# Kernel optimization log

Hardware: AMD Instinct MI355X
Metric: run time of the kernel (lower is better)

The kernel has to match this reference:

```python
import jax, jax.numpy as jnp
import numpy as np

B, T, D, H, HD, FF = 1024, 128, 128, 4, 32, 512
SCALE = D ** -0.5  # NOTE: original scales by full EMBED_DIM**-0.5, not head_dim
EPS = 1e-5


def setup_inputs() -> dict:
    key = jax.random.key(0)
    ks = jax.random.split(key, 14)
    s = 0.02
    return {
        "x": jax.random.normal(ks[0], (B, T, D), dtype=jnp.float32),
        "ln1_g": jnp.ones((D,), jnp.float32),
        "ln1_b": jnp.zeros((D,), jnp.float32),
        "Wq": jax.random.normal(ks[1], (H, HD, D), jnp.float32) * s,
        "Wk": jax.random.normal(ks[2], (H, HD, D), jnp.float32) * s,
        "Wv": jax.random.normal(ks[3], (H, HD, D), jnp.float32) * s,
        "Wo": jax.random.normal(ks[4], (D, D), jnp.float32) * s,
        "bo": jnp.zeros((D,), jnp.float32),
        "ln2_g": jnp.ones((D,), jnp.float32),
        "ln2_b": jnp.zeros((D,), jnp.float32),
        "W1": jax.random.normal(ks[5], (FF, D), jnp.float32) * s,
        "b1": jnp.zeros((FF,), jnp.float32),
        "W2": jax.random.normal(ks[6], (D, FF), jnp.float32) * s,
        "b2": jnp.zeros((D,), jnp.float32),
    }


def _layer_norm(x, g, b):
    mu = jnp.mean(x, axis=-1, keepdims=True)
    var = jnp.mean(jnp.square(x - mu), axis=-1, keepdims=True)
    return (x - mu) * jax.lax.rsqrt(var + EPS) * g + b


def reference(x, ln1_g, ln1_b, Wq, Wk, Wv, Wo, bo, ln2_g, ln2_b, W1, b1, W2, b2):
    # --- attention sub-block ---
    h = _layer_norm(x, ln1_g, ln1_b)                       # [B,T,D]
    q = jnp.einsum('btd,nhd->bnth', h, Wq)                 # [B,H,T,HD]
    k = jnp.einsum('btd,nhd->bnth', h, Wk)
    v = jnp.einsum('btd,nhd->bnth', h, Wv)
    scores = jnp.einsum('bnth,bnsh->bnts', q, k) * SCALE   # [B,H,T,T]
    causal = jnp.tril(jnp.ones((T, T), dtype=bool))
    scores = jnp.where(causal, scores, -jnp.inf)
    w = jax.nn.softmax(scores, axis=-1)                    # dropout = eval identity
    attn = jnp.einsum('bnts,bnsh->bnth', w, v)             # [B,H,T,HD]
    attn = attn.transpose(0, 2, 1, 3).reshape(B, T, D)     # concat heads
    x = x + attn @ Wo.T + bo
    # --- feed-forward sub-block ---
    h2 = _layer_norm(x, ln2_g, ln2_b)
    ff = jax.nn.relu(h2 @ W1.T + b1) @ W2.T + b2
    return x + ff
```

## Files before the change

kernel.cpp:

```cpp
#include <hip/hip_runtime.h>
#include <hip/hip_bf16.h>


typedef short bf16x8 __attribute__((ext_vector_type(8)));
typedef float f32x4  __attribute__((ext_vector_type(4)));
typedef unsigned short u16;
typedef unsigned int   u32;

#define TT   128
#define DDIM 128
#define FFD  512
#define PIT  136

#define QSC 0.12751744f

#if defined(__has_builtin)
#if __has_builtin(__builtin_amdgcn_exp2f)
#define EXP2F(x) __builtin_amdgcn_exp2f(x)
#else
#define EXP2F(x) exp2f(x)
#endif
#else
#define EXP2F(x) exp2f(x)
#endif

__device__ __forceinline__ u16 f2b(float f) {
    __hip_bfloat16 h = __float2bfloat16(f);
    return __builtin_bit_cast(u16, h);
}
__device__ __forceinline__ u32 pk2(float x, float y) {
    return (u32)f2b(x) | ((u32)f2b(y) << 16);
}
__device__ __forceinline__ void st_b64(u16* p, u32 lo, u32 hi) {
    uint2 v; v.x = lo; v.y = hi;
    *reinterpret_cast<uint2*>(p) = v;
}
__device__ __forceinline__ bf16x8 ldfrag(const u16* p) {
    return __builtin_bit_cast(bf16x8, *reinterpret_cast<const uint4*>(p));
}
__device__ __forceinline__ bf16x8 ldfrag_f32(const float* p) {
    float4 a = *reinterpret_cast<const float4*>(p);
    float4 b = *reinterpret_cast<const float4*>(p + 4);
    bf16x8 r;
    r[0] = (short)f2b(a.x); r[1] = (short)f2b(a.y);
    r[2] = (short)f2b(a.z); r[3] = (short)f2b(a.w);
    r[4] = (short)f2b(b.x); r[5] = (short)f2b(b.y);
    r[6] = (short)f2b(b.z); r[7] = (short)f2b(b.w);
    return r;
}
__device__ __forceinline__ f32x4 mfma16(bf16x8 a, bf16x8 b, f32x4 c) {
    return __builtin_amdgcn_mfma_f32_16x16x32_bf16(a, b, c, 0, 0, 0);
}

__global__ __launch_bounds__(512, 2) void tblock_kernel(
    const float* __restrict__ x,
    const float* __restrict__ ln1g, const float* __restrict__ ln1b,
    const float* __restrict__ Wq,   const float* __restrict__ Wk, const float* __restrict__ Wv,
    const float* __restrict__ Wo,   const float* __restrict__ bo,
    const float* __restrict__ ln2g, const float* __restrict__ ln2b,
    const float* __restrict__ W1,   const float* __restrict__ b1,
    const float* __restrict__ W2,   const float* __restrict__ b2,
    float* __restrict__ out)
{
    __shared__ __align__(16) u16 sm[4 * TT * PIT];
    u16* bufA = sm;
    u16* bufB = sm + 1 * TT * PIT;
    u16* bufC = sm + 2 * TT * PIT;
    u16* bufD = sm + 3 * TT * PIT;

    const int b    = blockIdx.x;
    const int tid  = threadIdx.x;
    const int w    = tid >> 6;
    const int l    = tid & 63;
    const int lq   = l & 15;
    const int quad = l >> 4;
    const float* xb = x + (size_t)b * (TT * DDIM);

    {
        const int row = tid >> 2, part = tid & 3;
        const float* src = xb + row * DDIM + part * 32;
        float v[32];
        float s = 0.f, s2 = 0.f;
        #pragma unroll
        for (int i = 0; i < 8; i++) {
            float4 u = *reinterpret_cast<const float4*>(src + i * 4);
            v[i * 4 + 0] = u.x; v[i * 4 + 1] = u.y;
            v[i * 4 + 2] = u.z; v[i * 4 + 3] = u.w;
            s  += u.x + u.y + u.z + u.w;
            s2 += u.x * u.x + u.y * u.y + u.z * u.z + u.w * u.w;
        }
        s  += __shfl_xor(s, 1);  s2 += __shfl_xor(s2, 1);
        s  += __shfl_xor(s, 2);  s2 += __shfl_xor(s2, 2);
        float mean = s * (1.f / 128.f);
        float var  = fmaxf(s2 * (1.f / 128.f) - mean * mean, 0.f);
        float rstd = rsqrtf(var + 1e-5f);
        u16* dst = bufA + row * PIT + part * 32;
        #pragma unroll
        for (int i = 0; i < 4; i++) {
            u32 o4[4];
            #pragma unroll
            for (int j = 0; j < 4; j++) {
                int c = part * 32 + i * 8 + 2 * j;
                float r0 = (v[i * 8 + 2 * j]     - mean) * rstd * ln1g[c]     + ln1b[c];
                float r1 = (v[i * 8 + 2 * j + 1] - mean) * rstd * ln1g[c + 1] + ln1b[c + 1];
                o4[j] = (u32)f2b(r0) | ((u32)f2b(r1) << 16);
            }
            uint4 pk; pk.x = o4[0]; pk.y = o4[1]; pk.z = o4[2]; pk.w = o4[3];
            *reinterpret_cast<uint4*>(dst + i * 8) = pk;
        }
    }
    __syncthreads();

    {
        bf16x8 aq[4], ak[4];
        #pragma unroll
        for (int ks = 0; ks < 4; ks++) {
            aq[ks] = ldfrag_f32(Wq + (w * 16 + lq) * DDIM + ks * 32 + quad * 8);
            ak[ks] = ldfrag_f32(Wk + (w * 16 + lq) * DDIM + ks * 32 + quad * 8);
        }
        #pragma unroll
        for (int m = 0; m < 8; m++) {
            f32x4 accq = {0, 0, 0, 0}, acck = {0, 0, 0, 0};
            #pragma unroll
            for (int ks = 0; ks < 4; ks++) {
                bf16x8 bh = ldfrag(bufA + (m * 16 + lq) * PIT + ks * 32 + quad * 8);
                accq = mfma16(aq[ks], bh, accq);
                acck = mfma16(ak[ks], bh, acck);
            }
            int t = m * 16 + lq;
            st_b64(bufB + t * PIT + w * 16 + quad * 4, pk2(accq[0], accq[1]), pk2(accq[2], accq[3]));
            st_b64(bufC + t * PIT + w * 16 + quad * 4, pk2(acck[0], acck[1]), pk2(acck[2], acck[3]));
        }
        bf16x8 av[4];
        #pragma unroll
        for (int ks = 0; ks < 4; ks++)
            av[ks] = ldfrag_f32(Wv + (w * 16 + lq) * DDIM + ks * 32 + quad * 8);
        #pragma unroll
        for (int n = 0; n < 8; n++) {
            f32x4 acc = {0, 0, 0, 0};
            #pragma unroll
            for (int ks = 0; ks < 4; ks++) {
                bf16x8 bh = ldfrag(bufA + (n * 16 + lq) * PIT + ks * 32 + quad * 8);
                acc = mfma16(av[ks], bh, acc);
            }
            #pragma unroll
            for (int r = 0; r < 4; r++) {
                int o = w * 16 + quad * 4 + r;
                bufD[o * PIT + n * 16 + lq] = f2b(acc[r]);
            }
        }
    }
    __syncthreads();

    const int trow = w * 16 + lq;
    #pragma unroll 1
    for (int h = 0; h < 4; h++) {
        bf16x8 qb = ldfrag(bufB + trow * PIT + h * 32 + quad * 8);
        float p[8][4];
        #pragma unroll
        for (int n = 0; n < 8; n++) {
            bf16x8 ka = ldfrag(bufC + (n * 16 + lq) * PIT + h * 32 + quad * 8);
            f32x4 s4 = mfma16(ka, qb, f32x4{0, 0, 0, 0});
            #pragma unroll
            for (int r = 0; r < 4; r++) p[n][r] = s4[r];
        }
        float mx = -3.0e38f;
        #pragma unroll
        for (int n = 0; n < 8; n++) {
            #pragma unroll
            for (int r = 0; r < 4; r++) {
                int sc = n * 16 + quad * 4 + r;
                float q = p[n][r] * QSC;
                p[n][r] = q;
                mx = (sc <= trow) ? fmaxf(mx, q) : mx;
            }
        }
        mx = fmaxf(mx, __shfl_xor(mx, 16));
        mx = fmaxf(mx, __shfl_xor(mx, 32));
        float sum = 0.f;
        #pragma unroll
        for (int n = 0; n < 8; n++) {
            float e[4];
            #pragma unroll
            for (int r = 0; r < 4; r++) {
                int sc = n * 16 + quad * 4 + r;
                e[r] = (sc <= trow) ? EXP2F(p[n][r] - mx) : 0.f;
                sum += e[r];
            }
            st_b64(bufA + trow * PIT + n * 16 + quad * 4, pk2(e[0], e[1]), pk2(e[2], e[3]));
        }
        sum += __shfl_xor(sum, 16);
        sum += __shfl_xor(sum, 32);
        float inv = 1.f / sum;
        asm volatile("s_waitcnt lgkmcnt(0)" ::: "memory");
        __builtin_amdgcn_sched_barrier(0);
        f32x4 o0 = {0, 0, 0, 0}, o1 = {0, 0, 0, 0};
        #pragma unroll
        for (int ks = 0; ks < 4; ks++) {
            bf16x8 pb  = ldfrag(bufA + trow * PIT + ks * 32 + quad * 8);
            bf16x8 va0 = ldfrag(bufD + (h * 32 + lq) * PIT + ks * 32 + quad * 8);
            bf16x8 va1 = ldfrag(bufD + (h * 32 + 16 + lq) * PIT + ks * 32 + quad * 8);
            o0 = mfma16(va0, pb, o0);
            o1 = mfma16(va1, pb, o1);
        }
        #pragma unroll
        for (int r = 0; r < 4; r++) { o0[r] *= inv; o1[r] *= inv; }
        st_b64(bufB + trow * PIT + h * 32 + quad * 4,      pk2(o0[0], o0[1]), pk2(o0[2], o0[3]));
        st_b64(bufB + trow * PIT + h * 32 + 16 + quad * 4, pk2(o1[0], o1[1]), pk2(o1[2], o1[3]));
    }
    __syncthreads();

    float x1res[8][4];
    {
        bf16x8 woa[4];
        #pragma unroll
        for (int ks = 0; ks < 4; ks++)
            woa[ks] = ldfrag_f32(Wo + (w * 16 + lq) * DDIM + ks * 32 + quad * 8);
        const float4 bo4 = *reinterpret_cast<const float4*>(bo + w * 16 + quad * 4);
        #pragma unroll
        for (int m = 0; m < 8; m++) {
            f32x4 acc = {0, 0, 0, 0};
            #pragma unroll
            for (int ks = 0; ks < 4; ks++) {
                bf16x8 ab = ldfrag(bufB + (m * 16 + lq) * PIT + ks * 32 + quad * 8);
                acc = mfma16(woa[ks], ab, acc);
            }
            int t = m * 16 + lq;
            const float4 xv = *reinterpret_cast<const float4*>(xb + t * DDIM + w * 16 + quad * 4);
            float v0 = acc[0] + xv.x + bo4.x;
            float v1 = acc[1] + xv.y + bo4.y;
            float v2 = acc[2] + xv.z + bo4.z;
            float v3 = acc[3] + xv.w + bo4.w;
            x1res[m][0] = v0; x1res[m][1] = v1; x1res[m][2] = v2; x1res[m][3] = v3;
            st_b64(bufC + t * PIT + w * 16 + quad * 4, pk2(v0, v1), pk2(v2, v3));
        }
    }
    __syncthreads();

    {
        const int row = tid >> 2, part = tid & 3;
        const u16* src = bufC + row * PIT + part * 32;
        float v[32];
        float s = 0.f, s2 = 0.f;
        #pragma unroll
        for (int i = 0; i < 4; i++) {
            uint4 u = *reinterpret_cast<const uint4*>(src + i * 8);
            u32 arr[4] = {u.x, u.y, u.z, u.w};
            #pragma unroll
            for (int j = 0; j < 4; j++) {
                float f0 = __uint_as_float((arr[j] & 0xffffu) << 16);
                float f1 = __uint_as_float(arr[j] & 0xffff0000u);
                v[i * 8 + 2 * j] = f0; v[i * 8 + 2 * j + 1] = f1;
                s += f0 + f1; s2 += f0 * f0 + f1 * f1;
            }
        }
        s  += __shfl_xor(s, 1);  s2 += __shfl_xor(s2, 1);
        s  += __shfl_xor(s, 2);  s2 += __shfl_xor(s2, 2);
        float mean = s * (1.f / 128.f);
        float var  = fmaxf(s2 * (1.f / 128.f) - mean * mean, 0.f);
        float rstd = rsqrtf(var + 1e-5f);
        u16* dst = bufD + row * PIT + part * 32;
        #pragma unroll
        for (int i = 0; i < 4; i++) {
            u32 o4[4];
            #pragma unroll
            for (int j = 0; j < 4; j++) {
                int c = part * 32 + i * 8 + 2 * j;
                float r0 = (v[i * 8 + 2 * j]     - mean) * rstd * ln2g[c]     + ln2b[c];
                float r1 = (v[i * 8 + 2 * j + 1] - mean) * rstd * ln2g[c + 1] + ln2b[c + 1];
                o4[j] = (u32)f2b(r0) | ((u32)f2b(r1) << 16);
            }
            uint4 pk; pk.x = o4[0]; pk.y = o4[1]; pk.z = o4[2]; pk.w = o4[3];
            *reinterpret_cast<uint4*>(dst + i * 8) = pk;
        }
    }
    __syncthreads();

    f32x4 oacc[8];
    #pragma unroll
    for (int m = 0; m < 8; m++) oacc[m] = f32x4{0, 0, 0, 0};

    #pragma unroll 1
    for (int fc = 0; fc < 4; fc++) {
        const int fbase = fc * 128;
        u16* gbuf = (fc & 1) ? bufB : bufA;
        bf16x8 w1a[4];
        #pragma unroll
        for (int ks = 0; ks < 4; ks++)
            w1a[ks] = ldfrag_f32(W1 + (fbase + w * 16 + lq) * DDIM + ks * 32 + quad * 8);
        const float4 b14 = *reinterpret_cast<const float4*>(b1 + fbase + w * 16 + quad * 4);
        #pragma unroll
        for (int m = 0; m < 8; m++) {
            f32x4 acc = {0, 0, 0, 0};
            #pragma unroll
            for (int ks = 0; ks < 4; ks++) {
                bf16x8 hb = ldfrag(bufD + (m * 16 + lq) * PIT + ks * 32 + quad * 8);
                acc = mfma16(w1a[ks], hb, acc);
            }
            int t = m * 16 + lq;
            float g0 = fmaxf(acc[0] + b14.x, 0.f);
            float g1 = fmaxf(acc[1] + b14.y, 0.f);
            float g2 = fmaxf(acc[2] + b14.z, 0.f);
            float g3 = fmaxf(acc[3] + b14.w, 0.f);
            st_b64(gbuf + t * PIT + w * 16 + quad * 4, pk2(g0, g1), pk2(g2, g3));
        }
        __syncthreads();
        bf16x8 w2a[4];
        #pragma unroll
        for (int ks = 0; ks < 4; ks++)
            w2a[ks] = ldfrag_f32(W2 + (w * 16 + lq) * FFD + fbase + ks * 32 + quad * 8);
        #pragma unroll
        for (int m = 0; m < 8; m++) {
            #pragma unroll
            for (int ks = 0; ks < 4; ks++) {
                bf16x8 gb = ldfrag(gbuf + (m * 16 + lq) * PIT + ks * 32 + quad * 8);
                oacc[m] = mfma16(w2a[ks], gb, oacc[m]);
            }
        }
    }

    {
        const float4 b24 = *reinterpret_cast<const float4*>(b2 + w * 16 + quad * 4);
        float* ob = out + (size_t)b * (TT * DDIM);
        #pragma unroll
        for (int m = 0; m < 8; m++) {
            int t = m * 16 + lq;
            float4 o;
            o.x = oacc[m][0] + x1res[m][0] + b24.x;
            o.y = oacc[m][1] + x1res[m][1] + b24.y;
            o.z = oacc[m][2] + x1res[m][2] + b24.z;
            o.w = oacc[m][3] + x1res[m][3] + b24.w;
            *reinterpret_cast<float4*>(ob + t * DDIM + w * 16 + quad * 4) = o;
        }
    }
}

extern "C" void kernel_launch(void* const* d_in, const int* in_sizes, int n_in,
                              void* d_out, int out_size, void* d_ws, size_t ws_size,
                              hipStream_t stream) {
    const float* x    = (const float*)d_in[0];
    const float* ln1g = (const float*)d_in[1];
    const float* ln1b = (const float*)d_in[2];
    const float* Wq   = (const float*)d_in[3];
    const float* Wk   = (const float*)d_in[4];
    const float* Wv   = (const float*)d_in[5];
    const float* Wo   = (const float*)d_in[6];
    const float* bo   = (const float*)d_in[7];
    const float* ln2g = (const float*)d_in[8];
    const float* ln2b = (const float*)d_in[9];
    const float* W1   = (const float*)d_in[10];
    const float* b1   = (const float*)d_in[11];
    const float* W2   = (const float*)d_in[12];
    const float* b2   = (const float*)d_in[13];
    float* out = (float*)d_out;

    const int nblocks = in_sizes[0] / (TT * DDIM);
    tblock_kernel<<<dim3(nblocks), dim3(512), 0, stream>>>(
        x, ln1g, ln1b, Wq, Wk, Wv, Wo, bo, ln2g, ln2b, W1, b1, W2, b2, out);
}
```

Baseline: 312.8 us.

## Pre-convert weights to bf16 and keep LN1/Q/softmax tiles in registers

A small prep kernel now converts all weight matrices to bf16 in the workspace once per call, so the main kernel no longer loads fp32 weights and converts them per block. LN1 output and Q (pre-scaled) stay in registers as MFMA fragments, and softmax probabilities are redistributed through cross-lane shuffles instead of a round trip through LDS. This cuts shared memory from four 128x136 bf16 buffers to two, which could raise occupancy. In exchange it adds a second kernel launch, more shuffle instructions and extra barriers in the attention and FFN loops.

```diff
diff --git a/kernel.cpp b/kernel.cpp
--- a/kernel.cpp
+++ b/kernel.cpp
@@ -11,6 +11,14 @@
 #define DDIM 128
 #define FFD  512
 #define PIT  136
+
+#define OWQ 0
+#define OWK 16384
+#define OWV 32768
+#define OWO 49152
+#define OW1 65536
+#define OW2 131072
+#define WTOT 196608
 
 #define QSC 0.12751744f
 
@@ -38,35 +46,71 @@
 __device__ __forceinline__ bf16x8 ldfrag(const u16* p) {
     return __builtin_bit_cast(bf16x8, *reinterpret_cast<const uint4*>(p));
 }
-__device__ __forceinline__ bf16x8 ldfrag_f32(const float* p) {
-    float4 a = *reinterpret_cast<const float4*>(p);
-    float4 b = *reinterpret_cast<const float4*>(p + 4);
-    bf16x8 r;
-    r[0] = (short)f2b(a.x); r[1] = (short)f2b(a.y);
-    r[2] = (short)f2b(a.z); r[3] = (short)f2b(a.w);
-    r[4] = (short)f2b(b.x); r[5] = (short)f2b(b.y);
-    r[6] = (short)f2b(b.z); r[7] = (short)f2b(b.w);
-    return r;
-}
 __device__ __forceinline__ f32x4 mfma16(bf16x8 a, bf16x8 b, f32x4 c) {
     return __builtin_amdgcn_mfma_f32_16x16x32_bf16(a, b, c, 0, 0, 0);
+}
+
+__device__ __forceinline__ void quad_collect_pk(const u32 (&pkv)[8][2],
+                                                bf16x8 (&fr)[4], int lane) {
+    const int srcA = (lane & 15) + ((lane & 16) << 1);
+    const int srcB = srcA + 16;
+    const bool hi = (lane & 32) != 0;
+    #pragma unroll
+    for (int g = 0; g < 4; g++) {
+        u32 D00 = pkv[2*g][0],     D01 = pkv[2*g][1];
+        u32 D10 = pkv[2*g + 1][0], D11 = pkv[2*g + 1][1];
+        u32 a00 = (u32)__shfl((int)D00, srcA);
+        u32 a10 = (u32)__shfl((int)D10, srcA);
+        u32 a01 = (u32)__shfl((int)D01, srcA);
+        u32 a11 = (u32)__shfl((int)D11, srcA);
+        u32 b00 = (u32)__shfl((int)D00, srcB);
+        u32 b10 = (u32)__shfl((int)D10, srcB);
+        u32 b01 = (u32)__shfl((int)D01, srcB);
+        u32 b11 = (u32)__shfl((int)D11, srcB);
+        uint4 q;
+        q.x = hi ? a10 : a00;
+        q.y = hi ? a11 : a01;
+        q.z = hi ? b10 : b00;
+        q.w = hi ? b11 : b01;
+        fr[g] = __builtin_bit_cast(bf16x8, q);
+    }
+}
+
+__global__ __launch_bounds__(256) void wprep(
+    const float* __restrict__ wq, const float* __restrict__ wk,
+    const float* __restrict__ wv, const float* __restrict__ wo,
+    const float* __restrict__ w1, const float* __restrict__ w2,
+    u16* __restrict__ dst)
+{
+    int i = (blockIdx.x * 256 + threadIdx.x) * 8;
+    if (i >= WTOT) return;
+    const float* s; int off;
+    if      (i < OWK) { s = wq; off = i - OWQ; }
+    else if (i < OWV) { s = wk; off = i - OWK; }
+    else if (i < OWO) { s = wv; off = i - OWV; }
+    else if (i < OW1) { s = wo; off = i - OWO; }
+    else if (i < OW2) { s = w1; off = i - OW1; }
+    else              { s = w2; off = i - OW2; }
+    float4 a = *reinterpret_cast<const float4*>(s + off);
+    float4 b = *reinterpret_cast<const float4*>(s + off + 4);
+    uint4 o;
+    o.x = pk2(a.x, a.y); o.y = pk2(a.z, a.w);
+    o.z = pk2(b.x, b.y); o.w = pk2(b.z, b.w);
+    *reinterpret_cast<uint4*>(dst + i) = o;
 }
 
 __global__ __launch_bounds__(512, 2) void tblock_kernel(
     const float* __restrict__ x,
     const float* __restrict__ ln1g, const float* __restrict__ ln1b,
-    const float* __restrict__ Wq,   const float* __restrict__ Wk, const float* __restrict__ Wv,
-    const float* __restrict__ Wo,   const float* __restrict__ bo,
+    const u16*  __restrict__ wbf,
+    const float* __restrict__ bo,
     const float* __restrict__ ln2g, const float* __restrict__ ln2b,
-    const float* __restrict__ W1,   const float* __restrict__ b1,
-    const float* __restrict__ W2,   const float* __restrict__ b2,
+    const float* __restrict__ b1,   const float* __restrict__ b2,
     float* __restrict__ out)
 {
-    __shared__ __align__(16) u16 sm[4 * TT * PIT];
-    u16* bufA = sm;
-    u16* bufB = sm + 1 * TT * PIT;
-    u16* bufC = sm + 2 * TT * PIT;
-    u16* bufD = sm + 3 * TT * PIT;
+    __shared__ __align__(16) u16 sm[2 * TT * PIT];
+    u16* bufK = sm;
+    u16* bufV = sm + TT * PIT;
 
     const int b    = blockIdx.x;
     const int tid  = threadIdx.x;
@@ -74,139 +118,150 @@
     const int l    = tid & 63;
     const int lq   = l & 15;
     const int quad = l >> 4;
+    const int trow = w * 16 + lq;
     const float* xb = x + (size_t)b * (TT * DDIM);
 
+    const u16* wq = wbf + OWQ;
+    const u16* wk = wbf + OWK;
+    const u16* wv = wbf + OWV;
+    const u16* wo = wbf + OWO;
+    const u16* w1 = wbf + OW1;
+    const u16* w2 = wbf + OW2;
+
+    bf16x8 hf[4];
     {
-        const int row = tid >> 2, part = tid & 3;
-        const float* src = xb + row * DDIM + part * 32;
         float v[32];
         float s = 0.f, s2 = 0.f;
         #pragma unroll
-        for (int i = 0; i < 8; i++) {
-            float4 u = *reinterpret_cast<const float4*>(src + i * 4);
-            v[i * 4 + 0] = u.x; v[i * 4 + 1] = u.y;
-            v[i * 4 + 2] = u.z; v[i * 4 + 3] = u.w;
-            s  += u.x + u.y + u.z + u.w;
-            s2 += u.x * u.x + u.y * u.y + u.z * u.z + u.w * u.w;
-        }
-        s  += __shfl_xor(s, 1);  s2 += __shfl_xor(s2, 1);
-        s  += __shfl_xor(s, 2);  s2 += __shfl_xor(s2, 2);
+        for (int ks = 0; ks < 4; ks++) {
+            const float* src = xb + trow * DDIM + ks * 32 + quad * 8;
+            float4 u0 = *reinterpret_cast<const float4*>(src);
+            float4 u1 = *reinterpret_cast<const float4*>(src + 4);
+            v[ks*8+0]=u0.x; v[ks*8+1]=u0.y; v[ks*8+2]=u0.z; v[ks*8+3]=u0.w;
+            v[ks*8+4]=u1.x; v[ks*8+5]=u1.y; v[ks*8+6]=u1.z; v[ks*8+7]=u1.w;
+            s  += u0.x+u0.y+u0.z+u0.w + u1.x+u1.y+u1.z+u1.w;
+            s2 += u0.x*u0.x+u0.y*u0.y+u0.z*u0.z+u0.w*u0.w
+                + u1.x*u1.x+u1.y*u1.y+u1.z*u1.z+u1.w*u1.w;
+        }
+        s  += __shfl_xor(s, 16);  s2 += __shfl_xor(s2, 16);
+        s  += __shfl_xor(s, 32);  s2 += __shfl_xor(s2, 32);
         float mean = s * (1.f / 128.f);
         float var  = fmaxf(s2 * (1.f / 128.f) - mean * mean, 0.f);
         float rstd = rsqrtf(var + 1e-5f);
-        u16* dst = bufA + row * PIT + part * 32;
-        #pragma unroll
-        for (int i = 0; i < 4; i++) {
-            u32 o4[4];
-            #pragma unroll
-            for (int j = 0; j < 4; j++) {
-                int c = part * 32 + i * 8 + 2 * j;
-                float r0 = (v[i * 8 + 2 * j]     - mean) * rstd * ln1g[c]     + ln1b[c];
-                float r1 = (v[i * 8 + 2 * j + 1] - mean) * rstd * ln1g[c + 1] + ln1b[c + 1];
-                o4[j] = (u32)f2b(r0) | ((u32)f2b(r1) << 16);
-            }
-            uint4 pk; pk.x = o4[0]; pk.y = o4[1]; pk.z = o4[2]; pk.w = o4[3];
-            *reinterpret_cast<uint4*>(dst + i * 8) = pk;
-        }
+        #pragma unroll
+        for (int ks = 0; ks < 4; ks++) {
+            const float* gp = ln1g + ks * 32 + quad * 8;
+            const float* bp = ln1b + ks * 32 + quad * 8;
+            float4 g0 = *reinterpret_cast<const float4*>(gp);
+            float4 g1 = *reinterpret_cast<const float4*>(gp + 4);
+            float4 c0 = *reinterpret_cast<const float4*>(bp);
+            float4 c1 = *reinterpret_cast<const float4*>(bp + 4);
+            float gg[8] = {g0.x,g0.y,g0.z,g0.w,g1.x,g1.y,g1.z,g1.w};
+            float bb[8] = {c0.x,c0.y,c0.z,c0.w,c1.x,c1.y,c1.z,c1.w};
+            #pragma unroll
+            for (int j = 0; j < 8; j++)
+                hf[ks][j] = (short)f2b((v[ks*8+j] - mean) * rstd * gg[j] + bb[j]);
+        }
+    }
+
+    #pragma unroll
+    for (int mt = 0; mt < 8; mt++) {
+        f32x4 acc = {0, 0, 0, 0};
+        #pragma unroll
+        for (int ks = 0; ks < 4; ks++) {
+            bf16x8 aw = ldfrag(wk + (mt * 16 + lq) * DDIM + ks * 32 + quad * 8);
+            acc = mfma16(aw, hf[ks], acc);
+        }
+        st_b64(bufK + trow * PIT + mt * 16 + quad * 4,
+               pk2(acc[0], acc[1]), pk2(acc[2], acc[3]));
+    }
+    bf16x8 qf[4];
+    {
+        u32 qpk[8][2];
+        #pragma unroll
+        for (int mt = 0; mt < 8; mt++) {
+            f32x4 acc = {0, 0, 0, 0};
+            #pragma unroll
+            for (int ks = 0; ks < 4; ks++) {
+                bf16x8 aw = ldfrag(wq + (mt * 16 + lq) * DDIM + ks * 32 + quad * 8);
+                acc = mfma16(aw, hf[ks], acc);
+            }
+            qpk[mt][0] = pk2(acc[0] * QSC, acc[1] * QSC);
+            qpk[mt][1] = pk2(acc[2] * QSC, acc[3] * QSC);
+        }
+        quad_collect_pk(qpk, qf, l);
+    }
+    #pragma unroll
+    for (int mt = 0; mt < 8; mt++) {
+        f32x4 acc = {0, 0, 0, 0};
+        #pragma unroll
+        for (int ks = 0; ks < 4; ks++) {
+            bf16x8 av = ldfrag(wv + (mt * 16 + lq) * DDIM + ks * 32 + quad * 8);
+            acc = mfma16(av, hf[ks], acc);
+        }
+        #pragma unroll
+        for (int r = 0; r < 4; r++)
+            bufV[(mt * 16 + quad * 4 + r) * PIT + trow] = f2b(acc[r]);
     }
     __syncthreads();
 
-    {
-        bf16x8 aq[4], ak[4];
-        #pragma unroll
-        for (int ks = 0; ks < 4; ks++) {
-            aq[ks] = ldfrag_f32(Wq + (w * 16 + lq) * DDIM + ks * 32 + quad * 8);
-            ak[ks] = ldfrag_f32(Wk + (w * 16 + lq) * DDIM + ks * 32 + quad * 8);
-        }
-        #pragma unroll
-        for (int m = 0; m < 8; m++) {
-            f32x4 accq = {0, 0, 0, 0}, acck = {0, 0, 0, 0};
-            #pragma unroll
-            for (int ks = 0; ks < 4; ks++) {
-                bf16x8 bh = ldfrag(bufA + (m * 16 + lq) * PIT + ks * 32 + quad * 8);
-                accq = mfma16(aq[ks], bh, accq);
-                acck = mfma16(ak[ks], bh, acck);
-            }
-            int t = m * 16 + lq;
-            st_b64(bufB + t * PIT + w * 16 + quad * 4, pk2(accq[0], accq[1]), pk2(accq[2], accq[3]));
-            st_b64(bufC + t * PIT + w * 16 + quad * 4, pk2(acck[0], acck[1]), pk2(acck[2], acck[3]));
-        }
-        bf16x8 av[4];
-        #pragma unroll
-        for (int ks = 0; ks < 4; ks++)
-            av[ks] = ldfrag_f32(Wv + (w * 16 + lq) * DDIM + ks * 32 + quad * 8);
+    #pragma unroll
+    for (int h = 0; h < 4; h++) {
+        float p[8][4];
         #pragma unroll
         for (int n = 0; n < 8; n++) {
-            f32x4 acc = {0, 0, 0, 0};
-            #pragma unroll
-            for (int ks = 0; ks < 4; ks++) {
-                bf16x8 bh = ldfrag(bufA + (n * 16 + lq) * PIT + ks * 32 + quad * 8);
-                acc = mfma16(av[ks], bh, acc);
-            }
-            #pragma unroll
-            for (int r = 0; r < 4; r++) {
-                int o = w * 16 + quad * 4 + r;
-                bufD[o * PIT + n * 16 + lq] = f2b(acc[r]);
-            }
-        }
-    }
-    __syncthreads();
-
-    const int trow = w * 16 + lq;
-    #pragma unroll 1
-    for (int h = 0; h < 4; h++) {
-        bf16x8 qb = ldfrag(bufB + trow * PIT + h * 32 + quad * 8);
-        float p[8][4];
-        #pragma unroll
-        for (int n = 0; n < 8; n++) {
-            bf16x8 ka = ldfrag(bufC + (n * 16 + lq) * PIT + h * 32 + quad * 8);
-            f32x4 s4 = mfma16(ka, qb, f32x4{0, 0, 0, 0});
+            bf16x8 ka = ldfrag(bufK + (n * 16 + lq) * PIT + h * 32 + quad * 8);
+            f32x4 s4 = mfma16(ka, qf[h], f32x4{0, 0, 0, 0});
             #pragma unroll
             for (int r = 0; r < 4; r++) p[n][r] = s4[r];
         }
+        __syncthreads();
         float mx = -3.0e38f;
         #pragma unroll
         for (int n = 0; n < 8; n++) {
             #pragma unroll
             for (int r = 0; r < 4; r++) {
                 int sc = n * 16 + quad * 4 + r;
-                float q = p[n][r] * QSC;
-                p[n][r] = q;
-                mx = (sc <= trow) ? fmaxf(mx, q) : mx;
+                mx = (sc <= trow) ? fmaxf(mx, p[n][r]) : mx;
             }
         }
         mx = fmaxf(mx, __shfl_xor(mx, 16));
         mx = fmaxf(mx, __shfl_xor(mx, 32));
         float sum = 0.f;
+        u32 ppk[8][2];
         #pragma unroll
         for (int n = 0; n < 8; n++) {
-            float e[4];
-            #pragma unroll
-            for (int r = 0; r < 4; r++) {
-                int sc = n * 16 + quad * 4 + r;
-                e[r] = (sc <= trow) ? EXP2F(p[n][r] - mx) : 0.f;
-                sum += e[r];
-            }
-            st_b64(bufA + trow * PIT + n * 16 + quad * 4, pk2(e[0], e[1]), pk2(e[2], e[3]));
+            float e0, e1, e2, e3;
+            {
+                int sc = n * 16 + quad * 4;
+                e0 = (sc     <= trow) ? EXP2F(p[n][0] - mx) : 0.f;
+                e1 = (sc + 1 <= trow) ? EXP2F(p[n][1] - mx) : 0.f;
+                e2 = (sc + 2 <= trow) ? EXP2F(p[n][2] - mx) : 0.f;
+                e3 = (sc + 3 <= trow) ? EXP2F(p[n][3] - mx) : 0.f;
+            }
+            sum += e0 + e1 + e2 + e3;
+            ppk[n][0] = pk2(e0, e1);
+            ppk[n][1] = pk2(e2, e3);
         }
         sum += __shfl_xor(sum, 16);
         sum += __shfl_xor(sum, 32);
         float inv = 1.f / sum;
-        asm volatile("s_waitcnt lgkmcnt(0)" ::: "memory");
-        __builtin_amdgcn_sched_barrier(0);
+        bf16x8 pfr[4];
+        quad_collect_pk(ppk, pfr, l);
         f32x4 o0 = {0, 0, 0, 0}, o1 = {0, 0, 0, 0};
         #pragma unroll
         for (int ks = 0; ks < 4; ks++) {
-            bf16x8 pb  = ldfrag(bufA + trow * PIT + ks * 32 + quad * 8);
-            bf16x8 va0 = ldfrag(bufD + (h * 32 + lq) * PIT + ks * 32 + quad * 8);
-            bf16x8 va1 = ldfrag(bufD + (h * 32 + 16 + lq) * PIT + ks * 32 + quad * 8);
-            o0 = mfma16(va0, pb, o0);
-            o1 = mfma16(va1, pb, o1);
+            bf16x8 va0 = ldfrag(bufV + (h * 32 + lq) * PIT + ks * 32 + quad * 8);
+            bf16x8 va1 = ldfrag(bufV + (h * 32 + 16 + lq) * PIT + ks * 32 + quad * 8);
+            o0 = mfma16(va0, pfr[ks], o0);
+            o1 = mfma16(va1, pfr[ks], o1);
         }
         #pragma unroll
         for (int r = 0; r < 4; r++) { o0[r] *= inv; o1[r] *= inv; }
-        st_b64(bufB + trow * PIT + h * 32 + quad * 4,      pk2(o0[0], o0[1]), pk2(o0[2], o0[3]));
-        st_b64(bufB + trow * PIT + h * 32 + 16 + quad * 4, pk2(o1[0], o1[1]), pk2(o1[2], o1[3]));
+        st_b64(bufK + trow * PIT + h * 32 + quad * 4,
+               pk2(o0[0], o0[1]), pk2(o0[2], o0[3]));
+        st_b64(bufK + trow * PIT + h * 32 + 16 + quad * 4,
+               pk2(o1[0], o1[1]), pk2(o1[2], o1[3]));
     }
     __syncthreads();
 
@@ -215,14 +270,14 @@
         bf16x8 woa[4];
         #pragma unroll
         for (int ks = 0; ks < 4; ks++)
-            woa[ks] = ldfrag_f32(Wo + (w * 16 + lq) * DDIM + ks * 32 + quad * 8);
+            woa[ks] = ldfrag(wo + (w * 16 + lq) * DDIM + ks * 32 + quad * 8);
         const float4 bo4 = *reinterpret_cast<const float4*>(bo + w * 16 + quad * 4);
         #pragma unroll
         for (int m = 0; m < 8; m++) {
             f32x4 acc = {0, 0, 0, 0};
             #pragma unroll
             for (int ks = 0; ks < 4; ks++) {
-                bf16x8 ab = ldfrag(bufB + (m * 16 + lq) * PIT + ks * 32 + quad * 8);
+                bf16x8 ab = ldfrag(bufK + (m * 16 + lq) * PIT + ks * 32 + quad * 8);
                 acc = mfma16(woa[ks], ab, acc);
             }
             int t = m * 16 + lq;
@@ -232,14 +287,14 @@
             float v2 = acc[2] + xv.z + bo4.z;
             float v3 = acc[3] + xv.w + bo4.w;
             x1res[m][0] = v0; x1res[m][1] = v1; x1res[m][2] = v2; x1res[m][3] = v3;
-            st_b64(bufC + t * PIT + w * 16 + quad * 4, pk2(v0, v1), pk2(v2, v3));
+            st_b64(bufV + t * PIT + w * 16 + quad * 4, pk2(v0, v1), pk2(v2, v3));
         }
     }
     __syncthreads();
 
     {
         const int row = tid >> 2, part = tid & 3;
-        const u16* src = bufC + row * PIT + part * 32;
+        const u16* src = bufV + row * PIT + part * 32;
         float v[32];
         float s = 0.f, s2 = 0.f;
         #pragma unroll
@@ -259,7 +314,7 @@
         float mean = s * (1.f / 128.f);
         float var  = fmaxf(s2 * (1.f / 128.f) - mean * mean, 0.f);
         float rstd = rsqrtf(var + 1e-5f);
-        u16* dst = bufD + row * PIT + part * 32;
+        u16* dst = bufK + row * PIT + part * 32;
         #pragma unroll
         for (int i = 0; i < 4; i++) {
             u32 o4[4];
@@ -283,18 +338,17 @@
     #pragma unroll 1
     for (int fc = 0; fc < 4; fc++) {
         const int fbase = fc * 128;
-        u16* gbuf = (fc & 1) ? bufB : bufA;
         bf16x8 w1a[4];
         #pragma unroll
         for (int ks = 0; ks < 4; ks++)
-            w1a[ks] = ldfrag_f32(W1 + (fbase + w * 16 + lq) * DDIM + ks * 32 + quad * 8);
+            w1a[ks] = ldfrag(w1 + (fbase + w * 16 + lq) * DDIM + ks * 32 + quad * 8);
         const float4 b14 = *reinterpret_cast<const float4*>(b1 + fbase + w * 16 + quad * 4);
         #pragma unroll
         for (int m = 0; m < 8; m++) {
             f32x4 acc = {0, 0, 0, 0};
             #pragma unroll
             for (int ks = 0; ks < 4; ks++) {
-                bf16x8 hb = ldfrag(bufD + (m * 16 + lq) * PIT + ks * 32 + quad * 8);
+                bf16x8 hb = ldfrag(bufK + (m * 16 + lq) * PIT + ks * 32 + quad * 8);
                 acc = mfma16(w1a[ks], hb, acc);
             }
             int t = m * 16 + lq;
@@ -302,21 +356,22 @@
             float g1 = fmaxf(acc[1] + b14.y, 0.f);
             float g2 = fmaxf(acc[2] + b14.z, 0.f);
             float g3 = fmaxf(acc[3] + b14.w, 0.f);
-            st_b64(gbuf + t * PIT + w * 16 + quad * 4, pk2(g0, g1), pk2(g2, g3));
+            st_b64(bufV + t * PIT + w * 16 + quad * 4, pk2(g0, g1), pk2(g2, g3));
         }
         __syncthreads();
         bf16x8 w2a[4];
         #pragma unroll
         for (int ks = 0; ks < 4; ks++)
-            w2a[ks] = ldfrag_f32(W2 + (w * 16 + lq) * FFD + fbase + ks * 32 + quad * 8);
+            w2a[ks] = ldfrag(w2 + (w * 16 + lq) * FFD + fbase + ks * 32 + quad * 8);
         #pragma unroll
         for (int m = 0; m < 8; m++) {
             #pragma unroll
             for (int ks = 0; ks < 4; ks++) {
-                bf16x8 gb = ldfrag(gbuf + (m * 16 + lq) * PIT + ks * 32 + quad * 8);
+                bf16x8 gb = ldfrag(bufV + (m * 16 + lq) * PIT + ks * 32 + quad * 8);
                 oacc[m] = mfma16(w2a[ks], gb, oacc[m]);
             }
         }
+        if (fc < 3) __syncthreads();
     }
 
     {
@@ -353,8 +408,12 @@
     const float* W2   = (const float*)d_in[12];
     const float* b2   = (const float*)d_in[13];
     float* out = (float*)d_out;
+    u16* wbf = (u16*)d_ws;
+
+    wprep<<<dim3((WTOT / 8 + 255) / 256), dim3(256), 0, stream>>>(
+        Wq, Wk, Wv, Wo, W1, W2, wbf);
 
     const int nblocks = in_sizes[0] / (TT * DDIM);
     tblock_kernel<<<dim3(nblocks), dim3(512), 0, stream>>>(
-        x, ln1g, ln1b, Wq, Wk, Wv, Wo, bo, ln2g, ln2b, W1, b1, W2, b2, out);
-}
+        x, ln1g, ln1b, wbf, bo, ln2g, ln2b, b1, b2, out);
+}
```

New measurement: 353.3 us. +12.9%, slower.

## Pre-convert weights to bf16 once and keep softmax probabilities in registers

Applied to the files above, without the earlier changes.

A small prep kernel converts all weight matrices to bf16 in the workspace and folds the attention scale into Wq, so each block loads half the weight bytes and skips per-block conversion. The softmax probabilities now go from accumulator layout to MFMA operand layout through cross-lane shuffles instead of an LDS round trip and wait. The residual is seeded into the FFN accumulators, which frees the separate residual registers. The cost is an extra kernel launch and many shuffle instructions per head.

```diff
diff --git a/kernel.cpp b/kernel.cpp
--- a/kernel.cpp
+++ b/kernel.cpp
@@ -11,6 +11,14 @@
 #define DDIM 128
 #define FFD  512
 #define PIT  136
+
+#define OWQ 0
+#define OWK 16384
+#define OWV 32768
+#define OWO 49152
+#define OW1 65536
+#define OW2 131072
+#define WTOT 196608
 
 #define QSC 0.12751744f
 
@@ -38,28 +46,66 @@
 __device__ __forceinline__ bf16x8 ldfrag(const u16* p) {
     return __builtin_bit_cast(bf16x8, *reinterpret_cast<const uint4*>(p));
 }
-__device__ __forceinline__ bf16x8 ldfrag_f32(const float* p) {
-    float4 a = *reinterpret_cast<const float4*>(p);
-    float4 b = *reinterpret_cast<const float4*>(p + 4);
-    bf16x8 r;
-    r[0] = (short)f2b(a.x); r[1] = (short)f2b(a.y);
-    r[2] = (short)f2b(a.z); r[3] = (short)f2b(a.w);
-    r[4] = (short)f2b(b.x); r[5] = (short)f2b(b.y);
-    r[6] = (short)f2b(b.z); r[7] = (short)f2b(b.w);
-    return r;
-}
 __device__ __forceinline__ f32x4 mfma16(bf16x8 a, bf16x8 b, f32x4 c) {
     return __builtin_amdgcn_mfma_f32_16x16x32_bf16(a, b, c, 0, 0, 0);
+}
+
+__device__ __forceinline__ void quad_collect_pk(const u32 (&pkv)[8][2],
+                                                bf16x8 (&fr)[4], int lane) {
+    const int srcA = (lane & 15) + ((lane & 16) << 1);
+    const int srcB = srcA + 16;
+    const bool hi = (lane & 32) != 0;
+    #pragma unroll
+    for (int g = 0; g < 4; g++) {
+        u32 D00 = pkv[2*g][0],     D01 = pkv[2*g][1];
+        u32 D10 = pkv[2*g + 1][0], D11 = pkv[2*g + 1][1];
+        u32 a00 = (u32)__shfl((int)D00, srcA);
+        u32 a10 = (u32)__shfl((int)D10, srcA);
+        u32 a01 = (u32)__shfl((int)D01, srcA);
+        u32 a11 = (u32)__shfl((int)D11, srcA);
+        u32 b00 = (u32)__shfl((int)D00, srcB);
+        u32 b10 = (u32)__shfl((int)D10, srcB);
+        u32 b01 = (u32)__shfl((int)D01, srcB);
+        u32 b11 = (u32)__shfl((int)D11, srcB);
+        uint4 q;
+        q.x = hi ? a10 : a00;
+        q.y = hi ? a11 : a01;
+        q.z = hi ? b10 : b00;
+        q.w = hi ? b11 : b01;
+        fr[g] = __builtin_bit_cast(bf16x8, q);
+    }
+}
+
+__global__ __launch_bounds__(256) void wprep(
+    const float* __restrict__ wq, const float* __restrict__ wk,
+    const float* __restrict__ wv, const float* __restrict__ wo,
+    const float* __restrict__ w1, const float* __restrict__ w2,
+    u16* __restrict__ dst)
+{
+    int i = (blockIdx.x * 256 + threadIdx.x) * 8;
+    if (i >= WTOT) return;
+    const float* s; int off; float sc = 1.0f;
+    if      (i < OWK) { s = wq; off = i - OWQ; sc = QSC; }
+    else if (i < OWV) { s = wk; off = i - OWK; }
+    else if (i < OWO) { s = wv; off = i - OWV; }
+    else if (i < OW1) { s = wo; off = i - OWO; }
+    else if (i < OW2) { s = w1; off = i - OW1; }
+    else              { s = w2; off = i - OW2; }
+    float4 a = *reinterpret_cast<const float4*>(s + off);
+    float4 b = *reinterpret_cast<const float4*>(s + off + 4);
+    uint4 o;
+    o.x = pk2(a.x * sc, a.y * sc); o.y = pk2(a.z * sc, a.w * sc);
+    o.z = pk2(b.x * sc, b.y * sc); o.w = pk2(b.z * sc, b.w * sc);
+    *reinterpret_cast<uint4*>(dst + i) = o;
 }
 
 __global__ __launch_bounds__(512, 2) void tblock_kernel(
     const float* __restrict__ x,
     const float* __restrict__ ln1g, const float* __restrict__ ln1b,
-    const float* __restrict__ Wq,   const float* __restrict__ Wk, const float* __restrict__ Wv,
-    const float* __restrict__ Wo,   const float* __restrict__ bo,
+    const u16*  __restrict__ wbf,
+    const float* __restrict__ bo,
     const float* __restrict__ ln2g, const float* __restrict__ ln2b,
-    const float* __restrict__ W1,   const float* __restrict__ b1,
-    const float* __restrict__ W2,   const float* __restrict__ b2,
+    const float* __restrict__ b1,   const float* __restrict__ b2,
     float* __restrict__ out)
 {
     __shared__ __align__(16) u16 sm[4 * TT * PIT];
@@ -74,7 +120,15 @@
     const int l    = tid & 63;
     const int lq   = l & 15;
     const int quad = l >> 4;
+    const int trow = w * 16 + lq;
     const float* xb = x + (size_t)b * (TT * DDIM);
+
+    const u16* wq = wbf + OWQ;
+    const u16* wk = wbf + OWK;
+    const u16* wv = wbf + OWV;
+    const u16* wo = wbf + OWO;
+    const u16* w1 = wbf + OW1;
+    const u16* w2 = wbf + OW2;
 
     {
         const int row = tid >> 2, part = tid & 3;
@@ -115,8 +169,8 @@
         bf16x8 aq[4], ak[4];
         #pragma unroll
         for (int ks = 0; ks < 4; ks++) {
-            aq[ks] = ldfrag_f32(Wq + (w * 16 + lq) * DDIM + ks * 32 + quad * 8);
-            ak[ks] = ldfrag_f32(Wk + (w * 16 + lq) * DDIM + ks * 32 + quad * 8);
+            aq[ks] = ldfrag(wq + (w * 16 + lq) * DDIM + ks * 32 + quad * 8);
+            ak[ks] = ldfrag(wk + (w * 16 + lq) * DDIM + ks * 32 + quad * 8);
         }
         #pragma unroll
         for (int m = 0; m < 8; m++) {
@@ -134,7 +188,7 @@
         bf16x8 av[4];
         #pragma unroll
         for (int ks = 0; ks < 4; ks++)
-            av[ks] = ldfrag_f32(Wv + (w * 16 + lq) * DDIM + ks * 32 + quad * 8);
+            av[ks] = ldfrag(wv + (w * 16 + lq) * DDIM + ks * 32 + quad * 8);
         #pragma unroll
         for (int n = 0; n < 8; n++) {
             f32x4 acc = {0, 0, 0, 0};
@@ -152,7 +206,6 @@
     }
     __syncthreads();
 
-    const int trow = w * 16 + lq;
     #pragma unroll 1
     for (int h = 0; h < 4; h++) {
         bf16x8 qb = ldfrag(bufB + trow * PIT + h * 32 + quad * 8);
@@ -170,38 +223,36 @@
             #pragma unroll
             for (int r = 0; r < 4; r++) {
                 int sc = n * 16 + quad * 4 + r;
-                float q = p[n][r] * QSC;
-                p[n][r] = q;
-                mx = (sc <= trow) ? fmaxf(mx, q) : mx;
+                mx = (sc <= trow) ? fmaxf(mx, p[n][r]) : mx;
             }
         }
         mx = fmaxf(mx, __shfl_xor(mx, 16));
         mx = fmaxf(mx, __shfl_xor(mx, 32));
         float sum = 0.f;
+        u32 ppk[8][2];
         #pragma unroll
         for (int n = 0; n < 8; n++) {
-            float e[4];
-            #pragma unroll
-            for (int r = 0; r < 4; r++) {
-                int sc = n * 16 + quad * 4 + r;
-                e[r] = (sc <= trow) ? EXP2F(p[n][r] - mx) : 0.f;
-                sum += e[r];
-            }
-            st_b64(bufA + trow * PIT + n * 16 + quad * 4, pk2(e[0], e[1]), pk2(e[2], e[3]));
+            int sc = n * 16 + quad * 4;
+            float e0 = (sc     <= trow) ? EXP2F(p[n][0] - mx) : 0.f;
+            float e1 = (sc + 1 <= trow) ? EXP2F(p[n][1] - mx) : 0.f;
+            float e2 = (sc + 2 <= trow) ? EXP2F(p[n][2] - mx) : 0.f;
+            float e3 = (sc + 3 <= trow) ? EXP2F(p[n][3] - mx) : 0.f;
+            sum += e0 + e1 + e2 + e3;
+            ppk[n][0] = pk2(e0, e1);
+            ppk[n][1] = pk2(e2, e3);
         }
         sum += __shfl_xor(sum, 16);
         sum += __shfl_xor(sum, 32);
         float inv = 1.f / sum;
-        asm volatile("s_waitcnt lgkmcnt(0)" ::: "memory");
-        __builtin_amdgcn_sched_barrier(0);
+        bf16x8 pfr[4];
+        quad_collect_pk(ppk, pfr, l);
         f32x4 o0 = {0, 0, 0, 0}, o1 = {0, 0, 0, 0};
         #pragma unroll
         for (int ks = 0; ks < 4; ks++) {
-            bf16x8 pb  = ldfrag(bufA + trow * PIT + ks * 32 + quad * 8);
             bf16x8 va0 = ldfrag(bufD + (h * 32 + lq) * PIT + ks * 32 + quad * 8);
             bf16x8 va1 = ldfrag(bufD + (h * 32 + 16 + lq) * PIT + ks * 32 + quad * 8);
-            o0 = mfma16(va0, pb, o0);
-            o1 = mfma16(va1, pb, o1);
+            o0 = mfma16(va0, pfr[ks], o0);
+            o1 = mfma16(va1, pfr[ks], o1);
         }
         #pragma unroll
         for (int r = 0; r < 4; r++) { o0[r] *= inv; o1[r] *= inv; }
@@ -210,12 +261,12 @@
     }
     __syncthreads();
 
-    float x1res[8][4];
+    f32x4 oacc[8];
     {
         bf16x8 woa[4];
         #pragma unroll
         for (int ks = 0; ks < 4; ks++)
-            woa[ks] = ldfrag_f32(Wo + (w * 16 + lq) * DDIM + ks * 32 + quad * 8);
+            woa[ks] = ldfrag(wo + (w * 16 + lq) * DDIM + ks * 32 + quad * 8);
         const float4 bo4 = *reinterpret_cast<const float4*>(bo + w * 16 + quad * 4);
         #pragma unroll
         for (int m = 0; m < 8; m++) {
@@ -227,12 +278,12 @@
             }
             int t = m * 16 + lq;
             const float4 xv = *reinterpret_cast<const float4*>(xb + t * DDIM + w * 16 + quad * 4);
-            float v0 = acc[0] + xv.x + bo4.x;
-            float v1 = acc[1] + xv.y + bo4.y;
-            float v2 = acc[2] + xv.z + bo4.z;
-            float v3 = acc[3] + xv.w + bo4.w;
-            x1res[m][0] = v0; x1res[m][1] = v1; x1res[m][2] = v2; x1res[m][3] = v3;
-            st_b64(bufC + t * PIT + w * 16 + quad * 4, pk2(v0, v1), pk2(v2, v3));
+            oacc[m][0] = acc[0] + xv.x + bo4.x;
+            oacc[m][1] = acc[1] + xv.y + bo4.y;
+            oacc[m][2] = acc[2] + xv.z + bo4.z;
+            oacc[m][3] = acc[3] + xv.w + bo4.w;
+            st_b64(bufC + t * PIT + w * 16 + quad * 4,
+                   pk2(oacc[m][0], oacc[m][1]), pk2(oacc[m][2], oacc[m][3]));
         }
     }
     __syncthreads();
@@ -276,10 +327,6 @@
     }
     __syncthreads();
 
-    f32x4 oacc[8];
-    #pragma unroll
-    for (int m = 0; m < 8; m++) oacc[m] = f32x4{0, 0, 0, 0};
-
     #pragma unroll 1
     for (int fc = 0; fc < 4; fc++) {
         const int fbase = fc * 128;
@@ -287,7 +334,7 @@
         bf16x8 w1a[4];
         #pragma unroll
         for (int ks = 0; ks < 4; ks++)
-            w1a[ks] = ldfrag_f32(W1 + (fbase + w * 16 + lq) * DDIM + ks * 32 + quad * 8);
+            w1a[ks] = ldfrag(w1 + (fbase + w * 16 + lq) * DDIM + ks * 32 + quad * 8);
         const float4 b14 = *reinterpret_cast<const float4*>(b1 + fbase + w * 16 + quad * 4);
         #pragma unroll
         for (int m = 0; m < 8; m++) {
@@ -308,7 +355,7 @@
         bf16x8 w2a[4];
         #pragma unroll
         for (int ks = 0; ks < 4; ks++)
-            w2a[ks] = ldfrag_f32(W2 + (w * 16 + lq) * FFD + fbase + ks * 32 + quad * 8);
+            w2a[ks] = ldfrag(w2 + (w * 16 + lq) * FFD + fbase + ks * 32 + quad * 8);
         #pragma unroll
         for (int m = 0; m < 8; m++) {
             #pragma unroll
@@ -326,10 +373,10 @@
         for (int m = 0; m < 8; m++) {
             int t = m * 16 + lq;
             float4 o;
-            o.x = oacc[m][0] + x1res[m][0] + b24.x;
-            o.y = oacc[m][1] + x1res[m][1] + b24.y;
-            o.z = oacc[m][2] + x1res[m][2] + b24.z;
-            o.w = oacc[m][3] + x1res[m][3] + b24.w;
+            o.x = oacc[m][0] + b24.x;
+            o.y = oacc[m][1] + b24.y;
+            o.z = oacc[m][2] + b24.z;
+            o.w = oacc[m][3] + b24.w;
             *reinterpret_cast<float4*>(ob + t * DDIM + w * 16 + quad * 4) = o;
         }
     }
@@ -353,8 +400,12 @@
     const float* W2   = (const float*)d_in[12];
     const float* b2   = (const float*)d_in[13];
     float* out = (float*)d_out;
+    u16* wbf = (u16*)d_ws;
+
+    wprep<<<dim3((WTOT / 8 + 255) / 256), dim3(256), 0, stream>>>(
+        Wq, Wk, Wv, Wo, W1, W2, wbf);
 
     const int nblocks = in_sizes[0] / (TT * DDIM);
     tblock_kernel<<<dim3(nblocks), dim3(512), 0, stream>>>(
-        x, ln1g, ln1b, Wq, Wk, Wv, Wo, bo, ln2g, ln2b, W1, b1, W2, b2, out);
-}
+        x, ln1g, ln1b, wbf, bo, ln2g, ln2b, b1, b2, out);
+}
```

Result: faster. 283.6 us (-9.3%).
